# Optimization experiments

Measured on AMD Instinct MI355X. Metric: run time of the kernel, lower is better.

## Reference

```python
import jax, jax.numpy as jnp
import numpy as np

B, T, D, H = 4, 1024, 1024, 16
DK = D // H
SCALE = float(np.sqrt(DK))


def setup_inputs() -> dict:
    key = jax.random.key(0)
    ks = jax.random.split(key, 12)
    std = 1.0 / np.sqrt(D)
    inp = {
        "x": jax.random.normal(ks[0], (B, T, D), dtype=jnp.float32),
        "s2_distances": jax.random.uniform(ks[1], (B, T, T), dtype=jnp.float32),
        # causal mask: 1 where attention allowed (j <= i)
        "mask": jnp.broadcast_to(jnp.tril(jnp.ones((T, T), dtype=jnp.int32)), (B, T, T)),
        "Wq": jax.random.uniform(ks[2], (D, D), jnp.float32, -std, std),
        "bq": jax.random.uniform(ks[3], (D,), jnp.float32, -std, std),
        "Wk": jax.random.uniform(ks[4], (D, D), jnp.float32, -std, std),
        "bk": jax.random.uniform(ks[5], (D,), jnp.float32, -std, std),
        "Wv": jax.random.uniform(ks[6], (D, D), jnp.float32, -std, std),
        "bv": jax.random.uniform(ks[7], (D,), jnp.float32, -std, std),
        "Wo": jax.random.uniform(ks[8], (D, D), jnp.float32, -std, std),
        "bo": jax.random.uniform(ks[9], (D,), jnp.float32, -std, std),
        "spatial_weight": jnp.float32(0.5),
    }
    return inp


def reference(x, s2_distances, mask, Wq, bq, Wk, bk, Wv, bv, Wo, bo, spatial_weight):
    b, t, _ = x.shape
    # projections: torch nn.Linear is x @ W.T + b
    def proj(W, bias):
        y = jnp.einsum("btd,ed->bte", x, W) + bias
        return y.reshape(b, t, H, DK).transpose(0, 2, 1, 3)  # [B,H,T,dk]

    Q, K, V = proj(Wq, bq), proj(Wk, bk), proj(Wv, bv)
    # scores: QK^T/sqrt(dk) - |alpha| * dist  (dist broadcast over heads)
    scores = jnp.einsum("bhqd,bhkd->bhqk", Q, K) / SCALE
    scores = scores - jnp.abs(spatial_weight) * s2_distances[:, None, :, :]
    scores = jnp.where(mask[:, None, :, :] == 0, -jnp.inf, scores)
    probs = jax.nn.softmax(scores, axis=-1)
    out = jnp.einsum("bhqk,bhkd->bhqd", probs, V)
    out = out.transpose(0, 2, 1, 3).reshape(b, t, D)
    return jnp.einsum("btd,ed->bte", out, Wo) + bo
```

## Files before the change

kernel.cpp:

```cpp
#include <hip/hip_runtime.h>
#include <stdint.h>

#define Tt 1024
#define Dd 1024
#define Hh 16

typedef unsigned short u16;
typedef __attribute__((ext_vector_type(8))) short short8;
typedef __attribute__((ext_vector_type(4))) float f32x4;
typedef __attribute__((ext_vector_type(4))) unsigned short u16x4;

typedef const __attribute__((address_space(1))) uint32_t* gptr_t;
typedef __attribute__((address_space(3))) uint32_t* lptr_t;

#define QSCALE 0.18033688011112042f
#define LOG2E 1.4426950408889634f

static __device__ __forceinline__ u16 f2bf(float f) {
  union { float f; unsigned u; } x;
  x.f = f;
  unsigned u = x.u;
  return (u16)((u + 0x7fffu + ((u >> 16) & 1u)) >> 16);
}

static __device__ __forceinline__ u16 f2bf_fast(float f) {
  union { float f; unsigned u; } x;
  x.f = f;
  return (u16)((x.u + 0x8000u) >> 16);
}

static __device__ __forceinline__ float bf2f(u16 u) {
  union { unsigned u; float f; } x;
  x.u = ((unsigned)u) << 16;
  return x.f;
}

static __device__ __forceinline__ float fexp2(float x) {
#if __has_builtin(__builtin_amdgcn_exp2f)
  return __builtin_amdgcn_exp2f(x);
#else
  return exp2f(x);
#endif
}

__global__ __launch_bounds__(256) void cvt_kernel(
    const float* __restrict__ x, const float* __restrict__ wq,
    const float* __restrict__ wk, const float* __restrict__ wv,
    const float* __restrict__ wo, u16* __restrict__ xb, u16* __restrict__ wb) {
  size_t i = ((size_t)blockIdx.x * 256 + threadIdx.x) * 4;
  const size_t XN = (size_t)4 * 1024 * 1024;
  const float* src;
  u16* dst;
  size_t off;
  if (i < XN) {
    src = x; dst = xb; off = i;
  } else {
    size_t j = i - XN;
    int wi = (int)(j >> 20);
    src = (wi == 0) ? wq : (wi == 1) ? wk : (wi == 2) ? wv : wo;
    dst = wb + ((size_t)wi << 20);
    off = j & ((1u << 20) - 1);
  }
  float4 v = *(const float4*)(src + off);
  u16x4 o;
  o.x = f2bf(v.x); o.y = f2bf(v.y); o.z = f2bf(v.z); o.w = f2bf(v.w);
  *(u16x4*)(dst + off) = o;
}

static __device__ __forceinline__ void gemm_mainloop_db(
    const u16* __restrict__ A, const u16* __restrict__ W,
    u16* lds, int m0, int n0, f32x4 acc[2][4]) {
  const int t = threadIdx.x;
  const int w = t >> 6, l = t & 63;
  const int quad = l >> 4, l15 = l & 15;
  const int wm = (w >> 1) * 32, wn = (w & 1) * 64;
  const int srow = t >> 3;
  const int scol = ((l & 7) ^ ((l >> 3) & 7)) * 8;
  const u16* ga = A + (size_t)(m0 + srow) * Dd + scol;
  const u16* gb = W + (size_t)(n0 + srow) * Dd + scol;
  char* ldc = (char*)lds;
  const int xr = l15 & 7;

  auto stage = [&](int k0, int buf) {
    char* base = ldc + buf * 32768 + w * 1024;
#pragma unroll
    for (int i = 0; i < 2; i++) {
      __builtin_amdgcn_global_load_lds((gptr_t)(ga + k0 + (size_t)i * 64 * Dd),
                                       (lptr_t)(base + i * 8192), 16, 0, 0);
      __builtin_amdgcn_global_load_lds((gptr_t)(gb + k0 + (size_t)i * 64 * Dd),
                                       (lptr_t)(base + 16384 + i * 8192), 16, 0, 0);
    }
  };

  stage(0, 0);
#pragma unroll 1
  for (int it = 0; it < Dd / 64; it++) {
    const int buf = it & 1;
    __builtin_amdgcn_s_waitcnt(0);
    __syncthreads();
    if (it + 1 < Dd / 64) stage((it + 1) * 64, buf ^ 1);
    const u16* lA = lds + buf * 16384;
    const u16* lB = lA + 8192;
#pragma unroll
    for (int kk = 0; kk < 2; kk++) {
      short8 af[2], bfr[4];
#pragma unroll
      for (int mi = 0; mi < 2; mi++)
        af[mi] = *(const short8*)(lA + (wm + mi * 16 + l15) * 64 +
                                  (((kk * 4 + quad) ^ xr) * 8));
#pragma unroll
      for (int ni = 0; ni < 4; ni++)
        bfr[ni] = *(const short8*)(lB + (wn + ni * 16 + l15) * 64 +
                                   (((kk * 4 + quad) ^ xr) * 8));
#pragma unroll
      for (int mi = 0; mi < 2; mi++)
#pragma unroll
        for (int ni = 0; ni < 4; ni++)
          acc[mi][ni] = __builtin_amdgcn_mfma_f32_16x16x32_bf16(af[mi], bfr[ni], acc[mi][ni], 0, 0, 0);
    }
  }
}

__global__ __launch_bounds__(512) void gemm_qkv_kernel(
    const u16* __restrict__ xb, const u16* __restrict__ wb,
    const float* __restrict__ bq, const float* __restrict__ bk,
    const float* __restrict__ bv, u16* __restrict__ Q, u16* __restrict__ Kk,
    u16* __restrict__ Vt, const float* __restrict__ dist,
    const float* __restrict__ alphap, u16* __restrict__ biasb) {
  __shared__ u16 lds[2 * 16384];
  const int z = blockIdx.z;
  if (z == 3) {
    const float scl = -fabsf(alphap[0]) * LOG2E;
    const size_t idx = (size_t)(blockIdx.x * 8 + blockIdx.y) * 512 + threadIdx.x;
#pragma unroll
    for (int i = 0; i < 8; i++) {
      const size_t off = idx * 4 + (size_t)i * 524288;
      float4 v = *(const float4*)(dist + off);
      u16x4 o;
      o.x = f2bf(v.x * scl); o.y = f2bf(v.y * scl);
      o.z = f2bf(v.z * scl); o.w = f2bf(v.w * scl);
      *(u16x4*)(biasb + off) = o;
    }
    return;
  }
  const u16* W = wb + ((size_t)z << 20);
  const float* bias = (z == 0) ? bq : (z == 1) ? bk : bv;
  const int m0 = blockIdx.x * 128, n0 = blockIdx.y * 128;
  f32x4 acc[2][4];
#pragma unroll
  for (int i = 0; i < 2; i++)
#pragma unroll
    for (int j = 0; j < 4; j++) acc[i][j] = (f32x4){0.f, 0.f, 0.f, 0.f};
  gemm_mainloop_db(xb, W, lds, m0, n0, acc);
  const int t = threadIdx.x, w = t >> 6, l = t & 63, quad = l >> 4, l15 = l & 15;
  const int wm = (w >> 1) * 32, wn = (w & 1) * 64;
  u16* smem = lds;
  __syncthreads();
  const float scl = (z == 0) ? QSCALE : 1.0f;
  if (z < 2) {
#pragma unroll
    for (int mi = 0; mi < 2; mi++)
#pragma unroll
      for (int ni = 0; ni < 4; ni++) {
        const int n = wn + ni * 16 + l15;
        const float bn = bias[n0 + n];
#pragma unroll
        for (int r = 0; r < 4; r++) {
          const int m = wm + mi * 16 + quad * 4 + r;
          smem[m * 128 + n] = f2bf((acc[mi][ni][r] + bn) * scl);
        }
      }
  } else {
#pragma unroll
    for (int mi = 0; mi < 2; mi++)
#pragma unroll
      for (int ni = 0; ni < 4; ni++) {
        const int n = wn + ni * 16 + l15;
        const float bn = bias[n0 + n];
        u16x4 o;
        o.x = f2bf(acc[mi][ni][0] + bn);
        o.y = f2bf(acc[mi][ni][1] + bn);
        o.z = f2bf(acc[mi][ni][2] + bn);
        o.w = f2bf(acc[mi][ni][3] + bn);
        *(u16x4*)&smem[n * 128 + wm + mi * 16 + quad * 4] = o;
      }
  }
  __syncthreads();
  const int row = t >> 4;
  const int col = (t & 15) * 8;
  if (z < 2) {
    u16* out = (z == 0) ? Q : Kk;
#pragma unroll
    for (int it = 0; it < 4; it++) {
      const int rr = it * 32 + row;
      *(short8*)(out + (size_t)(m0 + rr) * Dd + n0 + col) = *(const short8*)&smem[rr * 128 + col];
    }
  } else {
    const int b2 = m0 >> 10, tt0 = m0 & (Tt - 1);
#pragma unroll
    for (int it = 0; it < 4; it++) {
      const int rr = it * 32 + row;
      *(short8*)(Vt + ((size_t)b2 * Dd + n0 + rr) * Tt + tt0 + col) = *(const short8*)&smem[rr * 128 + col];
    }
  }
}

__global__ __launch_bounds__(512) void gemm_out_kernel(
    const u16* __restrict__ Ao, const u16* __restrict__ Wo,
    const float* __restrict__ bo, float* __restrict__ out) {
  __shared__ u16 lds[2 * 12288];
  const int m0 = blockIdx.x * 128, n0 = blockIdx.y * 64;
  const int t = threadIdx.x, w = t >> 6, l = t & 63, quad = l >> 4, l15 = l & 15;
  const int srow = t >> 3;
  const int scol = ((l & 7) ^ ((l >> 3) & 7)) * 8;
  const u16* ga = Ao + (size_t)(m0 + srow) * Dd + scol;
  const u16* gb = Wo + (size_t)(n0 + srow) * Dd + scol;
  char* ldc = (char*)lds;
  const int xr = l15 & 7;
  f32x4 acc[4];
#pragma unroll
  for (int j = 0; j < 4; j++) acc[j] = (f32x4){0.f, 0.f, 0.f, 0.f};

  auto stage = [&](int k0, int buf) {
    char* base = ldc + buf * 24576 + w * 1024;
#pragma unroll
    for (int i = 0; i < 2; i++)
      __builtin_amdgcn_global_load_lds((gptr_t)(ga + k0 + (size_t)i * 64 * Dd),
                                       (lptr_t)(base + i * 8192), 16, 0, 0);
    __builtin_amdgcn_global_load_lds((gptr_t)(gb + k0),
                                     (lptr_t)(base + 16384), 16, 0, 0);
  };

  stage(0, 0);
#pragma unroll 1
  for (int it = 0; it < Dd / 64; it++) {
    const int buf = it & 1;
    __builtin_amdgcn_s_waitcnt(0);
    __syncthreads();
    if (it + 1 < Dd / 64) stage((it + 1) * 64, buf ^ 1);
    const u16* lA = lds + buf * 12288;
    const u16* lB = lA + 8192;
#pragma unroll
    for (int kk = 0; kk < 2; kk++) {
      const int cs = ((kk * 4 + quad) ^ xr) * 8;
      const short8 af = *(const short8*)(lA + (w * 16 + l15) * 64 + cs);
#pragma unroll
      for (int ni = 0; ni < 4; ni++) {
        const short8 bfr = *(const short8*)(lB + (ni * 16 + l15) * 64 + cs);
        acc[ni] = __builtin_amdgcn_mfma_f32_16x16x32_bf16(af, bfr, acc[ni], 0, 0, 0);
      }
    }
  }
#pragma unroll
  for (int ni = 0; ni < 4; ni++) {
    const int n = n0 + ni * 16 + l15;
    const float bn = bo[n];
#pragma unroll
    for (int r = 0; r < 4; r++) {
      const int m = m0 + w * 16 + quad * 4 + r;
      out[(size_t)m * Dd + n] = acc[ni][r] + bn;
    }
  }
}

__global__ __launch_bounds__(256) void attn_kernel(
    const u16* __restrict__ Q, const u16* __restrict__ Kk,
    const u16* __restrict__ Vt, const u16* __restrict__ biasb,
    u16* __restrict__ Oo) {
  __shared__ u16 lK[2][64 * 64];
  __shared__ u16 lV[2][64 * 64];
  __shared__ u16 lPp[4][16 * 64];
  const int t = threadIdx.x, w = t >> 6, l = t & 63, quad = l >> 4, l15 = l & 15;
  const int g = blockIdx.x >> 8;
  const int j = (blockIdx.x >> 6) & 3;
  const int bh = blockIdx.x & 63;
  const int qb = (g == 0) ? 15 - j : (g == 1) ? 8 + j : (g == 2) ? 7 - j : j;
  const int h = bh & (Hh - 1), b = bh >> 4;
  const int q0 = qb * 64;

  const int srow = w * 8 + (l >> 3);
  const int schunk = ((l & 7) ^ ((l >> 3) & 7)) * 8;
  const u16* gK = Kk + ((size_t)b * Tt + srow) * Dd + h * 64 + schunk;
  const u16* gV = Vt + ((size_t)b * Dd + h * 64 + srow) * Tt + schunk;
  char* lKc0 = (char*)&lK[0][0];
  char* lVc0 = (char*)&lV[0][0];
  const int wbase = w * 1024;

  auto stage = [&](int k0, int buf) {
#pragma unroll
    for (int i = 0; i < 2; i++) {
      __builtin_amdgcn_global_load_lds(
          (gptr_t)(gK + (size_t)(k0 + i * 32) * Dd),
          (lptr_t)(lKc0 + buf * 8192 + wbase + i * 4096), 16, 0, 0);
      __builtin_amdgcn_global_load_lds(
          (gptr_t)(gV + (size_t)(i * 32) * Tt + k0),
          (lptr_t)(lVc0 + buf * 8192 + wbase + i * 4096), 16, 0, 0);
    }
  };

  const int qrow = q0 + w * 16 + l15;
  const u16* Qp = Q + ((size_t)b * Tt + qrow) * Dd + h * 64 + quad * 8;
  const short8 qf0 = *(const short8*)Qp;
  const short8 qf1 = *(const short8*)(Qp + 32);
  const u16* bp = biasb + ((size_t)b * Tt + qrow) * Tt + quad * 4;

  const int xr = l15 & 7;
  u16* lpr = &lPp[w][l15 * 64];
  const int niter = qb + 1;

  f32x4 oacc[4];
#pragma unroll
  for (int dt = 0; dt < 4; dt++) oacc[dt] = (f32x4){0.f, 0.f, 0.f, 0.f};
  f32x4 lsum4 = (f32x4){0.f, 0.f, 0.f, 0.f};
  u16x4 bbA[4], bbB[4];

  stage(0, 0);
#pragma unroll
  for (int nt = 0; nt < 4; nt++) bbA[nt] = *(const u16x4*)(bp + nt * 16);

#pragma unroll 1
  for (int kt = 0; kt < niter; kt++) {
    const int buf = kt & 1;
    __builtin_amdgcn_s_waitcnt(0);
    __syncthreads();
    if (kt + 1 < niter) {
      stage((kt + 1) * 64, buf ^ 1);
#pragma unroll
      for (int nt = 0; nt < 4; nt++)
        bbB[nt] = *(const u16x4*)(bp + (kt + 1) * 64 + nt * 16);
    }
    f32x4 sacc[4];
#pragma unroll
    for (int nt = 0; nt < 4; nt++) {
#pragma unroll
      for (int r = 0; r < 4; r++) sacc[nt][r] = bf2f(bbA[nt][r]);
    }
#pragma unroll
    for (int ks = 0; ks < 2; ks++) {
      const short8 qf = ks ? qf1 : qf0;
      const int cs = ((ks * 4 + quad) ^ xr) * 8;
#pragma unroll
      for (int nt = 0; nt < 4; nt++) {
        const short8 kf = *(const short8*)&lK[buf][(nt * 16 + l15) * 64 + cs];
        sacc[nt] = __builtin_amdgcn_mfma_f32_16x16x32_bf16(kf, qf, sacc[nt], 0, 0, 0);
      }
    }
    if (kt == qb) {
      const int kbase = kt * 64 + quad * 4;
#pragma unroll
      for (int nt = 0; nt < 4; nt++) {
        u16x4 pk;
#pragma unroll
        for (int r = 0; r < 4; r++) {
          const float p = (kbase + nt * 16 + r <= qrow) ? fexp2(sacc[nt][r]) : 0.f;
          lsum4[nt] += p;
          pk[r] = f2bf_fast(p);
        }
        *(u16x4*)&lpr[((nt * 4 + quad) ^ (xr << 1)) * 4] = pk;
      }
    } else {
#pragma unroll
      for (int nt = 0; nt < 4; nt++) {
        u16x4 pk;
#pragma unroll
        for (int r = 0; r < 4; r++) {
          const float p = fexp2(sacc[nt][r]);
          lsum4[nt] += p;
          pk[r] = f2bf_fast(p);
        }
        *(u16x4*)&lpr[((nt * 4 + quad) ^ (xr << 1)) * 4] = pk;
      }
    }
#pragma unroll
    for (int ks = 0; ks < 2; ks++) {
      const int cs = ((ks * 4 + quad) ^ xr) * 8;
      const short8 pa = *(const short8*)&lpr[cs];
#pragma unroll
      for (int dt = 0; dt < 4; dt++) {
        const short8 vf = *(const short8*)&lV[buf][(dt * 16 + l15) * 64 + cs];
        oacc[dt] = __builtin_amdgcn_mfma_f32_16x16x32_bf16(pa, vf, oacc[dt], 0, 0, 0);
      }
    }
#pragma unroll
    for (int nt = 0; nt < 4; nt++) bbA[nt] = bbB[nt];
  }

  float lsum = (lsum4[0] + lsum4[1]) + (lsum4[2] + lsum4[3]);
  lsum += __shfl_xor(lsum, 16);
  lsum += __shfl_xor(lsum, 32);
  const float inv = 1.0f / lsum;
  float invq[4];
#pragma unroll
  for (int r = 0; r < 4; r++) invq[r] = __shfl(inv, quad * 4 + r);
#pragma unroll
  for (int dt = 0; dt < 4; dt++) {
#pragma unroll
    for (int r = 0; r < 4; r++) {
      Oo[((size_t)b * Tt + q0 + w * 16 + quad * 4 + r) * Dd + h * 64 + dt * 16 + l15] =
          f2bf(oacc[dt][r] * invq[r]);
    }
  }
}

extern "C" void kernel_launch(void* const* d_in, const int* in_sizes, int n_in,
                              void* d_out, int out_size, void* d_ws, size_t ws_size,
                              hipStream_t stream) {
  const float* x = (const float*)d_in[0];
  const float* dist = (const float*)d_in[1];
  const float* Wq = (const float*)d_in[3];
  const float* bq = (const float*)d_in[4];
  const float* Wk = (const float*)d_in[5];
  const float* bk = (const float*)d_in[6];
  const float* Wv = (const float*)d_in[7];
  const float* bv = (const float*)d_in[8];
  const float* Wo = (const float*)d_in[9];
  const float* bo = (const float*)d_in[10];
  const float* alphap = (const float*)d_in[11];

  char* ws = (char*)d_ws;
  u16* xb = (u16*)(ws);
  u16* wb = (u16*)(ws + ((size_t)8 << 20));
  u16* Qb = (u16*)(ws + ((size_t)16 << 20));
  u16* Kb = (u16*)(ws + ((size_t)24 << 20));
  u16* Vtb = (u16*)(ws + ((size_t)32 << 20));
  u16* biasb = (u16*)(ws + ((size_t)40 << 20));
  u16* Ob = xb;
  float* outp = (float*)d_out;

  cvt_kernel<<<8192, 256, 0, stream>>>(x, Wq, Wk, Wv, Wo, xb, wb);
  dim3 g1(32, 8, 4);
  gemm_qkv_kernel<<<g1, 512, 0, stream>>>(xb, wb, bq, bk, bv, Qb, Kb, Vtb,
                                          dist, alphap, biasb);
  attn_kernel<<<1024, 256, 0, stream>>>(Qb, Kb, Vtb, biasb, Ob);
  dim3 g2(32, 16);
  gemm_out_kernel<<<g2, 512, 0, stream>>>(Ob, wb + ((size_t)3 << 20), bo, outp);
}
```

Baseline: 190.6 us.

## Rewrite QKV GEMM with 256x256 tiles, 4-stage LDS pipeline and XCD-aware mapping

Replaces the 128x128 double-buffered QKV projection with 256x256 tiles per block, a 4-deep global_load_lds ring buffer with split A/B staging, and interleaved MFMA phases using s_setprio and explicit waitcnt/barrier scheduling. A flat 256-block grid maps GEMM tiles and the distance-bias conversion blocks by XCD so tiles sharing an x row band land on the same XCD. The goals are more data reuse per LDS byte, hidden load latency, and better L2 locality. The cost is heavy register use (128 accumulator floats per thread), which may cap occupancy, plus fragile hand-written vmcnt counting.

```diff
diff --git a/kernel.cpp b/kernel.cpp
--- a/kernel.cpp
+++ b/kernel.cpp
@@ -4,6 +4,7 @@
 #define Tt 1024
 #define Dd 1024
 #define Hh 16
+#define NT 32
 
 typedef unsigned short u16;
 typedef __attribute__((ext_vector_type(8))) short short8;
@@ -67,74 +68,22 @@
   *(u16x4*)(dst + off) = o;
 }
 
-static __device__ __forceinline__ void gemm_mainloop_db(
-    const u16* __restrict__ A, const u16* __restrict__ W,
-    u16* lds, int m0, int n0, f32x4 acc[2][4]) {
-  const int t = threadIdx.x;
-  const int w = t >> 6, l = t & 63;
-  const int quad = l >> 4, l15 = l & 15;
-  const int wm = (w >> 1) * 32, wn = (w & 1) * 64;
-  const int srow = t >> 3;
-  const int scol = ((l & 7) ^ ((l >> 3) & 7)) * 8;
-  const u16* ga = A + (size_t)(m0 + srow) * Dd + scol;
-  const u16* gb = W + (size_t)(n0 + srow) * Dd + scol;
-  char* ldc = (char*)lds;
-  const int xr = l15 & 7;
-
-  auto stage = [&](int k0, int buf) {
-    char* base = ldc + buf * 32768 + w * 1024;
-#pragma unroll
-    for (int i = 0; i < 2; i++) {
-      __builtin_amdgcn_global_load_lds((gptr_t)(ga + k0 + (size_t)i * 64 * Dd),
-                                       (lptr_t)(base + i * 8192), 16, 0, 0);
-      __builtin_amdgcn_global_load_lds((gptr_t)(gb + k0 + (size_t)i * 64 * Dd),
-                                       (lptr_t)(base + 16384 + i * 8192), 16, 0, 0);
-    }
-  };
-
-  stage(0, 0);
-#pragma unroll 1
-  for (int it = 0; it < Dd / 64; it++) {
-    const int buf = it & 1;
-    __builtin_amdgcn_s_waitcnt(0);
-    __syncthreads();
-    if (it + 1 < Dd / 64) stage((it + 1) * 64, buf ^ 1);
-    const u16* lA = lds + buf * 16384;
-    const u16* lB = lA + 8192;
-#pragma unroll
-    for (int kk = 0; kk < 2; kk++) {
-      short8 af[2], bfr[4];
-#pragma unroll
-      for (int mi = 0; mi < 2; mi++)
-        af[mi] = *(const short8*)(lA + (wm + mi * 16 + l15) * 64 +
-                                  (((kk * 4 + quad) ^ xr) * 8));
-#pragma unroll
-      for (int ni = 0; ni < 4; ni++)
-        bfr[ni] = *(const short8*)(lB + (wn + ni * 16 + l15) * 64 +
-                                   (((kk * 4 + quad) ^ xr) * 8));
-#pragma unroll
-      for (int mi = 0; mi < 2; mi++)
-#pragma unroll
-        for (int ni = 0; ni < 4; ni++)
-          acc[mi][ni] = __builtin_amdgcn_mfma_f32_16x16x32_bf16(af[mi], bfr[ni], acc[mi][ni], 0, 0, 0);
-    }
-  }
-}
-
-__global__ __launch_bounds__(512) void gemm_qkv_kernel(
+__global__ __launch_bounds__(512, 2) void qkv_fused_kernel(
     const u16* __restrict__ xb, const u16* __restrict__ wb,
     const float* __restrict__ bq, const float* __restrict__ bk,
     const float* __restrict__ bv, u16* __restrict__ Q, u16* __restrict__ Kk,
     u16* __restrict__ Vt, const float* __restrict__ dist,
     const float* __restrict__ alphap, u16* __restrict__ biasb) {
-  __shared__ u16 lds[2 * 16384];
-  const int z = blockIdx.z;
-  if (z == 3) {
+  __shared__ u16 lds[65536];
+  const int bid = blockIdx.x;
+  const int xcd = bid & 7, cslot = bid >> 3;
+  if (cslot >= 24) {
+    const int cid = xcd * 8 + (cslot - 24);
     const float scl = -fabsf(alphap[0]) * LOG2E;
-    const size_t idx = (size_t)(blockIdx.x * 8 + blockIdx.y) * 512 + threadIdx.x;
-#pragma unroll
-    for (int i = 0; i < 8; i++) {
-      const size_t off = idx * 4 + (size_t)i * 524288;
+    const size_t idx = (size_t)cid * 512 + threadIdx.x;
+#pragma unroll 4
+    for (int i = 0; i < 32; i++) {
+      const size_t off = idx * 4 + (size_t)i * 131072;
       float4 v = *(const float4*)(dist + off);
       u16x4 o;
       o.x = f2bf(v.x * scl); o.y = f2bf(v.y * scl);
@@ -143,64 +92,145 @@
     }
     return;
   }
+  const int gid = xcd * 24 + cslot;
+  const int mt = gid / 12, ny = gid - mt * 12;
+  const int z = ny >> 2;
+  const int m0 = mt * 256, nc = (ny & 3) * 256;
   const u16* W = wb + ((size_t)z << 20);
+
+  const int t = threadIdx.x, w = t >> 6, l = t & 63;
+  const int quad = l >> 4, l15 = l & 15;
+  const int wr = w >> 2, wn = w & 3;
+  char* ldc = (char*)lds;
+
+  const int srow = t >> 2;
+  const int scw = ((t & 3) ^ ((srow >> 1) & 3)) * 8;
+  const u16* gA = xb + (size_t)(m0 + srow) * Dd + scw;
+  const u16* gB = W + (size_t)(nc + srow) * Dd + scw;
+  const int lb = w * 1024;
+
+  auto stageA = [&](int kt, int u) {
+    __builtin_amdgcn_global_load_lds(
+        (gptr_t)(gA + (size_t)u * 128 * Dd + kt * 32),
+        (lptr_t)(ldc + (kt & 3) * 32768 + u * 8192 + lb), 16, 0, 0);
+  };
+  auto stageB = [&](int kt, int u) {
+    __builtin_amdgcn_global_load_lds(
+        (gptr_t)(gB + (size_t)u * 128 * Dd + kt * 32),
+        (lptr_t)(ldc + (kt & 3) * 32768 + 16384 + u * 8192 + lb), 16, 0, 0);
+  };
+
+  f32x4 acc[8][4];
+#pragma unroll
+  for (int i = 0; i < 8; i++)
+#pragma unroll
+    for (int j = 0; j < 4; j++) acc[i][j] = (f32x4){0.f, 0.f, 0.f, 0.f};
+
+#pragma unroll
+  for (int p = 0; p < 3; p++) {
+    stageA(p, 0); stageA(p, 1); stageB(p, 0); stageB(p, 1);
+  }
+  asm volatile("s_waitcnt vmcnt(8)" ::: "memory");
+  __builtin_amdgcn_s_barrier();
+
+  const int rsw = (quad ^ ((l15 >> 1) & 3)) * 16;
+  const int aoff = wr * 8192 + l15 * 64 + rsw;
+  const int boff = 16384 + wn * 4096 + l15 * 64 + rsw;
+
+#pragma unroll 1
+  for (int kt = 0; kt < NT; kt++) {
+    const char* sl = ldc + (kt & 3) * 32768;
+    short8 af[4], bfv[4];
+#pragma unroll
+    for (int i = 0; i < 4; i++) af[i] = *(const short8*)(sl + aoff + i * 1024);
+#pragma unroll
+    for (int i = 0; i < 4; i++) bfv[i] = *(const short8*)(sl + boff + i * 1024);
+    if (kt + 3 < NT) { stageA(kt + 3, 0); stageA(kt + 3, 1); }
+    __builtin_amdgcn_s_barrier();
+    asm volatile("s_waitcnt lgkmcnt(0)" ::: "memory");
+    __builtin_amdgcn_sched_barrier(0);
+    __builtin_amdgcn_s_setprio(1);
+#pragma unroll
+    for (int mi = 0; mi < 4; mi++)
+#pragma unroll
+      for (int ni = 0; ni < 4; ni++)
+        acc[mi][ni] = __builtin_amdgcn_mfma_f32_16x16x32_bf16(
+            af[mi], bfv[ni], acc[mi][ni], 0, 0, 0);
+    __builtin_amdgcn_s_setprio(0);
+    __builtin_amdgcn_s_barrier();
+#pragma unroll
+    for (int i = 0; i < 4; i++)
+      af[i] = *(const short8*)(sl + aoff + 4096 + i * 1024);
+    if (kt + 3 < NT) { stageB(kt + 3, 0); stageB(kt + 3, 1); }
+    if (kt < NT - 3) {
+      asm volatile("s_waitcnt vmcnt(8)" ::: "memory");
+    } else if (kt == NT - 3) {
+      asm volatile("s_waitcnt vmcnt(4)" ::: "memory");
+    } else if (kt == NT - 2) {
+      asm volatile("s_waitcnt vmcnt(0)" ::: "memory");
+    }
+    __builtin_amdgcn_s_barrier();
+    asm volatile("s_waitcnt lgkmcnt(0)" ::: "memory");
+    __builtin_amdgcn_sched_barrier(0);
+    __builtin_amdgcn_s_setprio(1);
+#pragma unroll
+    for (int mi = 0; mi < 4; mi++)
+#pragma unroll
+      for (int ni = 0; ni < 4; ni++)
+        acc[mi + 4][ni] = __builtin_amdgcn_mfma_f32_16x16x32_bf16(
+            af[mi], bfv[ni], acc[mi + 4][ni], 0, 0, 0);
+    __builtin_amdgcn_s_setprio(0);
+    __builtin_amdgcn_s_barrier();
+  }
+
   const float* bias = (z == 0) ? bq : (z == 1) ? bk : bv;
-  const int m0 = blockIdx.x * 128, n0 = blockIdx.y * 128;
-  f32x4 acc[2][4];
-#pragma unroll
-  for (int i = 0; i < 2; i++)
-#pragma unroll
-    for (int j = 0; j < 4; j++) acc[i][j] = (f32x4){0.f, 0.f, 0.f, 0.f};
-  gemm_mainloop_db(xb, W, lds, m0, n0, acc);
-  const int t = threadIdx.x, w = t >> 6, l = t & 63, quad = l >> 4, l15 = l & 15;
-  const int wm = (w >> 1) * 32, wn = (w & 1) * 64;
-  u16* smem = lds;
-  __syncthreads();
   const float scl = (z == 0) ? QSCALE : 1.0f;
   if (z < 2) {
 #pragma unroll
-    for (int mi = 0; mi < 2; mi++)
+    for (int mi = 0; mi < 8; mi++)
 #pragma unroll
       for (int ni = 0; ni < 4; ni++) {
-        const int n = wn + ni * 16 + l15;
-        const float bn = bias[n0 + n];
+        const int n = wn * 64 + ni * 16 + l15;
+        const float bn = bias[nc + n];
 #pragma unroll
         for (int r = 0; r < 4; r++) {
-          const int m = wm + mi * 16 + quad * 4 + r;
-          smem[m * 128 + n] = f2bf((acc[mi][ni][r] + bn) * scl);
+          const int m = wr * 128 + mi * 16 + quad * 4 + r;
+          lds[m * 256 + n] = f2bf((acc[mi][ni][r] + bn) * scl);
         }
       }
   } else {
 #pragma unroll
-    for (int mi = 0; mi < 2; mi++)
+    for (int mi = 0; mi < 8; mi++)
 #pragma unroll
       for (int ni = 0; ni < 4; ni++) {
-        const int n = wn + ni * 16 + l15;
-        const float bn = bias[n0 + n];
+        const int n = wn * 64 + ni * 16 + l15;
+        const float bn = bias[nc + n];
         u16x4 o;
         o.x = f2bf(acc[mi][ni][0] + bn);
         o.y = f2bf(acc[mi][ni][1] + bn);
         o.z = f2bf(acc[mi][ni][2] + bn);
         o.w = f2bf(acc[mi][ni][3] + bn);
-        *(u16x4*)&smem[n * 128 + wm + mi * 16 + quad * 4] = o;
+        *(u16x4*)&lds[n * 256 + wr * 128 + mi * 16 + quad * 4] = o;
       }
   }
   __syncthreads();
-  const int row = t >> 4;
-  const int col = (t & 15) * 8;
+  const int row = t >> 5;
+  const int chunk = (t & 31) * 8;
   if (z < 2) {
     u16* out = (z == 0) ? Q : Kk;
 #pragma unroll
-    for (int it = 0; it < 4; it++) {
-      const int rr = it * 32 + row;
-      *(short8*)(out + (size_t)(m0 + rr) * Dd + n0 + col) = *(const short8*)&smem[rr * 128 + col];
+    for (int it = 0; it < 16; it++) {
+      const int rr = it * 16 + row;
+      *(short8*)(out + (size_t)(m0 + rr) * Dd + nc + chunk) =
+          *(const short8*)&lds[rr * 256 + chunk];
     }
   } else {
-    const int b2 = m0 >> 10, tt0 = m0 & (Tt - 1);
-#pragma unroll
-    for (int it = 0; it < 4; it++) {
-      const int rr = it * 32 + row;
-      *(short8*)(Vt + ((size_t)b2 * Dd + n0 + rr) * Tt + tt0 + col) = *(const short8*)&smem[rr * 128 + col];
+    const int b2 = m0 >> 10, t0 = m0 & (Tt - 1);
+#pragma unroll
+    for (int it = 0; it < 16; it++) {
+      const int rr = it * 16 + row;
+      *(short8*)(Vt + ((size_t)b2 * Dd + nc + rr) * Tt + t0 + chunk) =
+          *(const short8*)&lds[rr * 256 + chunk];
     }
   }
 }
@@ -428,9 +458,8 @@
   float* outp = (float*)d_out;
 
   cvt_kernel<<<8192, 256, 0, stream>>>(x, Wq, Wk, Wv, Wo, xb, wb);
-  dim3 g1(32, 8, 4);
-  gemm_qkv_kernel<<<g1, 512, 0, stream>>>(xb, wb, bq, bk, bv, Qb, Kb, Vtb,
-                                          dist, alphap, biasb);
+  qkv_fused_kernel<<<256, 512, 0, stream>>>(xb, wb, bq, bk, bv, Qb, Kb, Vtb,
+                                            dist, alphap, biasb);
   attn_kernel<<<1024, 256, 0, stream>>>(Qb, Kb, Vtb, biasb, Ob);
   dim3 g2(32, 16);
   gemm_out_kernel<<<g2, 512, 0, stream>>>(Ob, wb + ((size_t)3 << 20), bo, outp);
```

Result: slower. 194.9 us (+2.3%).

## Fuse distance bias into attention and retile output GEMM with deeper pipelining

Applied to the files above, without the earlier changes.

Drops the separate pass that converted the distance matrix to scaled bf16 inside the QKV GEMM launch. The attention kernel now reads fp32 distances directly, scales them in registers, and prefetches two tiles ahead, using vmcnt-based waits in place of full waitcnt(0). The output GEMM moves to 128x128 tiles with a three-stage-style prefetch, split barriers and raised MFMA priority. The aim is to avoid writing and re-reading a bf16 bias tensor, at the cost of attention reading twice as many bytes of distance data.

```diff
diff --git a/kernel.cpp b/kernel.cpp
--- a/kernel.cpp
+++ b/kernel.cpp
@@ -27,12 +27,6 @@
   union { float f; unsigned u; } x;
   x.f = f;
   return (u16)((x.u + 0x8000u) >> 16);
-}
-
-static __device__ __forceinline__ float bf2f(u16 u) {
-  union { unsigned u; float f; } x;
-  x.u = ((unsigned)u) << 16;
-  return x.f;
 }
 
 static __device__ __forceinline__ float fexp2(float x) {
@@ -125,24 +119,9 @@
     const u16* __restrict__ xb, const u16* __restrict__ wb,
     const float* __restrict__ bq, const float* __restrict__ bk,
     const float* __restrict__ bv, u16* __restrict__ Q, u16* __restrict__ Kk,
-    u16* __restrict__ Vt, const float* __restrict__ dist,
-    const float* __restrict__ alphap, u16* __restrict__ biasb) {
+    u16* __restrict__ Vt) {
   __shared__ u16 lds[2 * 16384];
   const int z = blockIdx.z;
-  if (z == 3) {
-    const float scl = -fabsf(alphap[0]) * LOG2E;
-    const size_t idx = (size_t)(blockIdx.x * 8 + blockIdx.y) * 512 + threadIdx.x;
-#pragma unroll
-    for (int i = 0; i < 8; i++) {
-      const size_t off = idx * 4 + (size_t)i * 524288;
-      float4 v = *(const float4*)(dist + off);
-      u16x4 o;
-      o.x = f2bf(v.x * scl); o.y = f2bf(v.y * scl);
-      o.z = f2bf(v.z * scl); o.w = f2bf(v.w * scl);
-      *(u16x4*)(biasb + off) = o;
-    }
-    return;
-  }
   const u16* W = wb + ((size_t)z << 20);
   const float* bias = (z == 0) ? bq : (z == 1) ? bk : bv;
   const int m0 = blockIdx.x * 128, n0 = blockIdx.y * 128;
@@ -208,65 +187,98 @@
 __global__ __launch_bounds__(512) void gemm_out_kernel(
     const u16* __restrict__ Ao, const u16* __restrict__ Wo,
     const float* __restrict__ bo, float* __restrict__ out) {
-  __shared__ u16 lds[2 * 12288];
-  const int m0 = blockIdx.x * 128, n0 = blockIdx.y * 64;
-  const int t = threadIdx.x, w = t >> 6, l = t & 63, quad = l >> 4, l15 = l & 15;
-  const int srow = t >> 3;
-  const int scol = ((l & 7) ^ ((l >> 3) & 7)) * 8;
-  const u16* ga = Ao + (size_t)(m0 + srow) * Dd + scol;
-  const u16* gb = Wo + (size_t)(n0 + srow) * Dd + scol;
+  __shared__ u16 lds[32768];
+  const int mt = blockIdx.x & 31, ny = blockIdx.x >> 5;
+  const int m0 = mt * 128, n0 = ny * 128;
+  const int t = threadIdx.x, w = t >> 6, l = t & 63;
+  const int quad = l >> 4, l15 = l & 15;
+  const int wr = w >> 2, wn = w & 3;
   char* ldc = (char*)lds;
-  const int xr = l15 & 7;
-  f32x4 acc[4];
-#pragma unroll
-  for (int j = 0; j < 4; j++) acc[j] = (f32x4){0.f, 0.f, 0.f, 0.f};
-
-  auto stage = [&](int k0, int buf) {
-    char* base = ldc + buf * 24576 + w * 1024;
-#pragma unroll
-    for (int i = 0; i < 2; i++)
-      __builtin_amdgcn_global_load_lds((gptr_t)(ga + k0 + (size_t)i * 64 * Dd),
-                                       (lptr_t)(base + i * 8192), 16, 0, 0);
-    __builtin_amdgcn_global_load_lds((gptr_t)(gb + k0),
-                                     (lptr_t)(base + 16384), 16, 0, 0);
+
+  const int srow = w * 8 + (l >> 3);
+  const int schunk = ((l & 7) ^ ((l >> 3) & 7)) * 8;
+  const u16* gA = Ao + (size_t)(m0 + srow) * Dd + schunk;
+  const u16* gB = Wo + (size_t)(n0 + srow) * Dd + schunk;
+
+  auto stage = [&](int kt) {
+    char* base = ldc + (kt & 1) * 32768 + w * 1024;
+#pragma unroll
+    for (int i = 0; i < 2; i++) {
+      __builtin_amdgcn_global_load_lds(
+          (gptr_t)(gA + (size_t)i * 64 * Dd + (size_t)kt * 64),
+          (lptr_t)(base + i * 8192), 16, 0, 0);
+      __builtin_amdgcn_global_load_lds(
+          (gptr_t)(gB + (size_t)i * 64 * Dd + (size_t)kt * 64),
+          (lptr_t)(base + 16384 + i * 8192), 16, 0, 0);
+    }
   };
 
-  stage(0, 0);
+  f32x4 acc[4][2];
+#pragma unroll
+  for (int i = 0; i < 4; i++)
+#pragma unroll
+    for (int j = 0; j < 2; j++) acc[i][j] = (f32x4){0.f, 0.f, 0.f, 0.f};
+
+  stage(0); stage(1);
+  asm volatile("s_waitcnt vmcnt(4)" ::: "memory");
+  __builtin_amdgcn_s_barrier();
+
+  const int swl = l15 & 7;
+
 #pragma unroll 1
-  for (int it = 0; it < Dd / 64; it++) {
-    const int buf = it & 1;
-    __builtin_amdgcn_s_waitcnt(0);
-    __syncthreads();
-    if (it + 1 < Dd / 64) stage((it + 1) * 64, buf ^ 1);
-    const u16* lA = lds + buf * 12288;
-    const u16* lB = lA + 8192;
-#pragma unroll
-    for (int kk = 0; kk < 2; kk++) {
-      const int cs = ((kk * 4 + quad) ^ xr) * 8;
-      const short8 af = *(const short8*)(lA + (w * 16 + l15) * 64 + cs);
-#pragma unroll
-      for (int ni = 0; ni < 4; ni++) {
-        const short8 bfr = *(const short8*)(lB + (ni * 16 + l15) * 64 + cs);
-        acc[ni] = __builtin_amdgcn_mfma_f32_16x16x32_bf16(af, bfr, acc[ni], 0, 0, 0);
-      }
-    }
-  }
-#pragma unroll
-  for (int ni = 0; ni < 4; ni++) {
-    const int n = n0 + ni * 16 + l15;
-    const float bn = bo[n];
-#pragma unroll
-    for (int r = 0; r < 4; r++) {
-      const int m = m0 + w * 16 + quad * 4 + r;
-      out[(size_t)m * Dd + n] = acc[ni][r] + bn;
-    }
-  }
+  for (int kt = 0; kt < 16; kt++) {
+    const char* sl = ldc + (kt & 1) * 32768;
+    short8 af[2][4], bfv[2][2];
+#pragma unroll
+    for (int ks = 0; ks < 2; ks++) {
+      const int cs = ((ks * 4 + quad) ^ swl) * 16;
+#pragma unroll
+      for (int mi = 0; mi < 4; mi++)
+        af[ks][mi] = *(const short8*)(sl + (wr * 64 + mi * 16 + l15) * 128 + cs);
+#pragma unroll
+      for (int ni = 0; ni < 2; ni++)
+        bfv[ks][ni] = *(const short8*)(sl + 16384 + (wn * 32 + ni * 16 + l15) * 128 + cs);
+    }
+    __builtin_amdgcn_s_barrier();
+    if (kt + 2 < 16) stage(kt + 2);
+    asm volatile("s_waitcnt lgkmcnt(0)" ::: "memory");
+    __builtin_amdgcn_sched_barrier(0);
+    __builtin_amdgcn_s_setprio(1);
+#pragma unroll
+    for (int ks = 0; ks < 2; ks++)
+#pragma unroll
+      for (int mi = 0; mi < 4; mi++)
+#pragma unroll
+        for (int ni = 0; ni < 2; ni++)
+          acc[mi][ni] = __builtin_amdgcn_mfma_f32_16x16x32_bf16(
+              af[ks][mi], bfv[ks][ni], acc[mi][ni], 0, 0, 0);
+    __builtin_amdgcn_s_setprio(0);
+    if (kt < 14) {
+      asm volatile("s_waitcnt vmcnt(4)" ::: "memory");
+    } else if (kt == 14) {
+      asm volatile("s_waitcnt vmcnt(0)" ::: "memory");
+    }
+    if (kt < 15) __builtin_amdgcn_s_barrier();
+  }
+
+#pragma unroll
+  for (int mi = 0; mi < 4; mi++)
+#pragma unroll
+    for (int ni = 0; ni < 2; ni++) {
+      const int n = n0 + wn * 32 + ni * 16 + l15;
+      const float bn = bo[n];
+#pragma unroll
+      for (int r = 0; r < 4; r++) {
+        const int m = m0 + wr * 64 + mi * 16 + quad * 4 + r;
+        out[(size_t)m * Dd + n] = acc[mi][ni][r] + bn;
+      }
+    }
 }
 
 __global__ __launch_bounds__(256) void attn_kernel(
     const u16* __restrict__ Q, const u16* __restrict__ Kk,
-    const u16* __restrict__ Vt, const u16* __restrict__ biasb,
-    u16* __restrict__ Oo) {
+    const u16* __restrict__ Vt, const float* __restrict__ dist,
+    const float* __restrict__ alphap, u16* __restrict__ Oo) {
   __shared__ u16 lK[2][64 * 64];
   __shared__ u16 lV[2][64 * 64];
   __shared__ u16 lPp[4][16 * 64];
@@ -277,6 +289,7 @@
   const int qb = (g == 0) ? 15 - j : (g == 1) ? 8 + j : (g == 2) ? 7 - j : j;
   const int h = bh & (Hh - 1), b = bh >> 4;
   const int q0 = qb * 64;
+  const float scl = -fabsf(alphap[0]) * LOG2E;
 
   const int srow = w * 8 + (l >> 3);
   const int schunk = ((l & 7) ^ ((l >> 3) & 7)) * 8;
@@ -302,7 +315,7 @@
   const u16* Qp = Q + ((size_t)b * Tt + qrow) * Dd + h * 64 + quad * 8;
   const short8 qf0 = *(const short8*)Qp;
   const short8 qf1 = *(const short8*)(Qp + 32);
-  const u16* bp = biasb + ((size_t)b * Tt + qrow) * Tt + quad * 4;
+  const float* bp = dist + ((size_t)b * Tt + qrow) * Tt + quad * 4;
 
   const int xr = l15 & 7;
   u16* lpr = &lPp[w][l15 * 64];
@@ -312,28 +325,39 @@
 #pragma unroll
   for (int dt = 0; dt < 4; dt++) oacc[dt] = (f32x4){0.f, 0.f, 0.f, 0.f};
   f32x4 lsum4 = (f32x4){0.f, 0.f, 0.f, 0.f};
-  u16x4 bbA[4], bbB[4];
+  f32x4 bbA[4], bbB[4], bbC[4];
 
   stage(0, 0);
 #pragma unroll
-  for (int nt = 0; nt < 4; nt++) bbA[nt] = *(const u16x4*)(bp + nt * 16);
+  for (int nt = 0; nt < 4; nt++) bbA[nt] = *(const f32x4*)(bp + nt * 16);
+  if (niter > 1) {
+#pragma unroll
+    for (int nt = 0; nt < 4; nt++) bbB[nt] = *(const f32x4*)(bp + 64 + nt * 16);
+  } else {
+#pragma unroll
+    for (int nt = 0; nt < 4; nt++) bbB[nt] = bbA[nt];
+  }
 
 #pragma unroll 1
   for (int kt = 0; kt < niter; kt++) {
     const int buf = kt & 1;
-    __builtin_amdgcn_s_waitcnt(0);
-    __syncthreads();
     if (kt + 1 < niter) {
-      stage((kt + 1) * 64, buf ^ 1);
+      asm volatile("s_waitcnt vmcnt(4)" ::: "memory");
+    } else {
+      asm volatile("s_waitcnt vmcnt(0)" ::: "memory");
+    }
+    __builtin_amdgcn_s_barrier();
+    if (kt + 1 < niter) stage((kt + 1) * 64, buf ^ 1);
+    if (kt + 2 < niter) {
 #pragma unroll
       for (int nt = 0; nt < 4; nt++)
-        bbB[nt] = *(const u16x4*)(bp + (kt + 1) * 64 + nt * 16);
+        bbC[nt] = *(const f32x4*)(bp + (kt + 2) * 64 + nt * 16);
     }
     f32x4 sacc[4];
 #pragma unroll
     for (int nt = 0; nt < 4; nt++) {
 #pragma unroll
-      for (int r = 0; r < 4; r++) sacc[nt][r] = bf2f(bbA[nt][r]);
+      for (int r = 0; r < 4; r++) sacc[nt][r] = scl * bbA[nt][r];
     }
 #pragma unroll
     for (int ks = 0; ks < 2; ks++) {
@@ -382,7 +406,7 @@
       }
     }
 #pragma unroll
-    for (int nt = 0; nt < 4; nt++) bbA[nt] = bbB[nt];
+    for (int nt = 0; nt < 4; nt++) { bbA[nt] = bbB[nt]; bbB[nt] = bbC[nt]; }
   }
 
   float lsum = (lsum4[0] + lsum4[1]) + (lsum4[2] + lsum4[3]);
@@ -423,15 +447,12 @@
   u16* Qb = (u16*)(ws + ((size_t)16 << 20));
   u16* Kb = (u16*)(ws + ((size_t)24 << 20));
   u16* Vtb = (u16*)(ws + ((size_t)32 << 20));
-  u16* biasb = (u16*)(ws + ((size_t)40 << 20));
   u16* Ob = xb;
   float* outp = (float*)d_out;
 
   cvt_kernel<<<8192, 256, 0, stream>>>(x, Wq, Wk, Wv, Wo, xb, wb);
-  dim3 g1(32, 8, 4);
-  gemm_qkv_kernel<<<g1, 512, 0, stream>>>(xb, wb, bq, bk, bv, Qb, Kb, Vtb,
-                                          dist, alphap, biasb);
-  attn_kernel<<<1024, 256, 0, stream>>>(Qb, Kb, Vtb, biasb, Ob);
-  dim3 g2(32, 16);
-  gemm_out_kernel<<<g2, 512, 0, stream>>>(Ob, wb + ((size_t)3 << 20), bo, outp);
-}
+  dim3 g1(32, 8, 3);
+  gemm_qkv_kernel<<<g1, 512, 0, stream>>>(xb, wb, bq, bk, bv, Qb, Kb, Vtb);
+  attn_kernel<<<1024, 256, 0, stream>>>(Qb, Kb, Vtb, dist, alphap, Ob);
+  gemm_out_kernel<<<256, 512, 0, stream>>>(Ob, wb + ((size_t)3 << 20), bo, outp);
+}
```

After: 194.6 us. +2.1%, slower.
